# Kernel tuning notes

Measured on AMD Instinct MI355X. Metric: run time of the kernel, lower is better.

## Reference

```python
import jax, jax.numpy as jnp
import numpy as np

N, FEAT, PROP, HID, OUT = 8192, 128, 3, 256, 64
IN_SMOOTH = (PROP + 1) * FEAT  # 512
PRELU_INIT = 0.25


def prelu(x, a):
    return jnp.where(x > 0, x, a * x)


def setup_inputs() -> dict:
    key = jax.random.key(0)
    ks = jax.random.split(key, 12)
    s = 0.05
    return {
        "ori_feature": jax.random.normal(ks[0], (N, FEAT), jnp.float32),
        "smoothed_feature": jax.random.normal(ks[1], (N, IN_SMOOTH), jnp.float32),
        "processed_feature": jax.random.normal(ks[2], (N, IN_SMOOTH), jnp.float32),
        "universal_re": jax.random.normal(ks[3], (N, N), jnp.float32),
        # smooth-trans linears
        "Ws1": jax.random.normal(ks[4], (HID, IN_SMOOTH), jnp.float32) * s,
        "bs1": jnp.zeros((HID,), jnp.float32),
        "Ws2": jax.random.normal(ks[5], (OUT, HID), jnp.float32) * s,
        "bs2": jnp.zeros((OUT,), jnp.float32),
        # local-trans linears
        "Wl1": jax.random.normal(ks[6], (HID, FEAT), jnp.float32) * s,
        "bl1": jnp.zeros((HID,), jnp.float32),
        "Wl2": jax.random.normal(ks[7], (OUT, HID), jnp.float32) * s,
        "bl2": jnp.zeros((OUT,), jnp.float32),
        # hete-propagate-layer linears
        "Wh1": jax.random.normal(ks[8], (HID, IN_SMOOTH), jnp.float32) * s,
        "bh1": jnp.zeros((HID,), jnp.float32),
        "Wh2": jax.random.normal(ks[9], (OUT, HID), jnp.float32) * s,
        "bh2": jnp.zeros((OUT,), jnp.float32),
        # PReLU slopes (scalar, one per nn.PReLU())
        "a_model": jnp.float32(PRELU_INIT),
        "a_hete": jnp.float32(PRELU_INIT),
    }


def _getre_scale(emb):
    # emb: [N, OUT]
    es = jax.nn.softmax(emb, axis=1)
    re = es @ es.T                              # [N, N]
    d = jnp.diagonal(re)[:, None]               # [N, 1]
    scaling = d @ d.T                            # [N, N]
    re = re / jnp.maximum(jnp.sqrt(scaling), jnp.float32(1e-9))
    re = re - jnp.diag(jnp.diagonal(re))
    return re


def _forward(ori_feature, smoothed_feature, universal_re,
             Ws1, bs1, Ws2, bs2, Wl1, bl1, Wl2, bl2,
             Wh1, bh1, Wh2, bh2, a_model, a_hete):
    beta = jnp.float32(0.0)  # HetePropagateLayer default beta=0
    # smooth path (dropout is identity in eval)
    h = prelu(smoothed_feature @ Ws1.T + bs1, a_model)
    local_smooth_emb = h @ Ws2.T + bs2
    # local path
    g = prelu(ori_feature @ Wl1.T + bl1, a_model)
    local_ori_emb = g @ Wl2.T + bl2
    # hete propagation on input_prop_feature = smoothed_feature
    f = prelu(smoothed_feature @ Wh1.T + bh1, a_hete)
    feature_emb = f @ Wh2.T + bh2                # [N, OUT]
    re = _getre_scale(feature_emb)               # [N, N]
    lre = beta * universal_re + (1.0 - beta) * re
    m = jnp.mean(lre)
    M = jnp.max(lre)
    pos_diff = M - m                             # pos_min = 0
    shifted = lre - m
    # neg branch: -((shifted - (-m)) / (0 - (-m))) = -((shifted + m) / m)
    lre = jnp.where(shifted > 0, shifted / pos_diff, -((shifted + m) / m))
    # add_diag in source effectively adds identity to its input (bug preserved)
    lre = lre + jnp.eye(N, dtype=lre.dtype)
    pos_signal = prelu(lre, a_hete)
    neg_signal = prelu(-lre, a_hete)
    prop_pos = jax.nn.softmax(pos_signal @ feature_emb, axis=1)
    prop_neg = jax.nn.softmax(neg_signal @ feature_emb, axis=1)
    local_message_propagation = (prop_pos - prop_neg + feature_emb) / 2
    return local_ori_emb, local_smooth_emb, local_message_propagation


def reference(ori_feature, smoothed_feature, processed_feature, universal_re,
              Ws1, bs1, Ws2, bs2, Wl1, bl1, Wl2, bl2,
              Wh1, bh1, Wh2, bh2, a_model, a_hete):
    # processed_feature is unused in the original forward (only .to(device))
    return _forward(ori_feature, smoothed_feature, universal_re,
                    Ws1, bs1, Ws2, bs2, Wl1, bl1, Wl2, bl2,
                    Wh1, bh1, Wh2, bh2, a_model, a_hete)
```

## Files before the change

kernel.cpp:

```cpp
#include <hip/hip_runtime.h>
#include <hip/hip_bf16.h>

#define N 8192

typedef _Float16 half_t;
typedef __attribute__((ext_vector_type(8))) _Float16 half8;
typedef __attribute__((ext_vector_type(4))) float f32x4;
typedef unsigned int uint;
typedef unsigned short ushort;

#define MFMA16(a, b, c) __builtin_amdgcn_mfma_f32_16x16x32_f16(a, b, c, 0, 0, 0)

#define RES_SCALE 2048.0f
#define RES_INV   (1.0f / 2048.0f)

union UH8 { int4 i; half8 h; };
__device__ __forceinline__ half8 ldh(const ushort* p) {
    UH8 t; t.i = *(const int4*)p; return t.h;
}
__device__ __forceinline__ ushort h2u(half_t h) {
    union { half_t f; ushort u; } c; c.f = h; return c.u;
}

__device__ __forceinline__ float wave_max(float v) {
#pragma unroll
    for (int o = 32; o > 0; o >>= 1) v = fmaxf(v, __shfl_xor(v, o, 64));
    return v;
}
__device__ __forceinline__ float wave_sum(float v) {
#pragma unroll
    for (int o = 32; o > 0; o >>= 1) v += __shfl_xor(v, o, 64);
    return v;
}

__global__ __launch_bounds__(256) void split_f16(
    const float* __restrict__ X, ushort* __restrict__ Xh, ushort* __restrict__ Xl)
{
    const size_t i = ((size_t)blockIdx.x * 256 + threadIdx.x) * 4;
    float4 v = *(const float4*)(X + i);
    ushort h[4], l[4];
#pragma unroll
    for (int t = 0; t < 4; ++t) {
        float f = (&v.x)[t];
        half_t hh = (half_t)f;
        half_t ll = (half_t)((f - (float)hh) * RES_SCALE);
        h[t] = h2u(hh); l[t] = h2u(ll);
    }
    *(ushort4*)(Xh + i) = make_ushort4(h[0], h[1], h[2], h[3]);
    *(ushort4*)(Xl + i) = make_ushort4(l[0], l[1], l[2], l[3]);
}

__global__ __launch_bounds__(128) void gemm_f16s(
    const ushort* __restrict__ Ah, const ushort* __restrict__ Al,
    const ushort* __restrict__ Wh, const ushort* __restrict__ Wl,
    const float* __restrict__ bias, const float* __restrict__ slope_p,
    int Nc, int K, int act,
    float* __restrict__ Cf, ushort* __restrict__ Ch, ushort* __restrict__ Cl)
{
    const int w = threadIdx.x >> 6, lane = threadIdx.x & 63;
    const int l16 = lane & 15, lg = lane >> 4;
    const int row0 = blockIdx.x * 32 + w * 16;
    const int n0 = blockIdx.y * 64;
    f32x4 acc1[4], acc2[4];
#pragma unroll
    for (int c = 0; c < 4; ++c) {
        acc1[c] = (f32x4){0.f, 0.f, 0.f, 0.f};
        acc2[c] = (f32x4){0.f, 0.f, 0.f, 0.f};
    }
    for (int k0 = 0; k0 < K; k0 += 32) {
        const size_t aoff = (size_t)(row0 + l16) * K + lg * 8 + k0;
        half8 Af = ldh(Ah + aoff);
        half8 Alf = ldh(Al + aoff);
#pragma unroll
        for (int c = 0; c < 4; ++c) {
            const size_t woff = (size_t)(n0 + c * 16 + l16) * K + lg * 8 + k0;
            half8 Wf = ldh(Wh + woff);
            half8 Wlf = ldh(Wl + woff);
            acc1[c] = MFMA16(Af, Wf, acc1[c]);
            acc2[c] = MFMA16(Af, Wlf, acc2[c]);
            acc2[c] = MFMA16(Alf, Wf, acc2[c]);
        }
    }
    const float slope = *slope_p;
#pragma unroll
    for (int c = 0; c < 4; ++c) {
        const int col = n0 + c * 16 + l16;
        const float b = bias[col];
#pragma unroll
        for (int r = 0; r < 4; ++r) {
            const int row = row0 + lg * 4 + r;
            float v = fmaf(acc2[c][r], RES_INV, acc1[c][r]) + b;
            if (act) v = v > 0.f ? v : slope * v;
            const size_t off = (size_t)row * Nc + col;
            if (Cf) Cf[off] = v;
            if (Ch) {
                half_t hh = (half_t)v;
                half_t ll = (half_t)((v - (float)hh) * RES_SCALE);
                Ch[off] = h2u(hh); Cl[off] = h2u(ll);
            }
        }
    }
}

__global__ __launch_bounds__(256) void row_softmax_u(
    const float* __restrict__ E, ushort* __restrict__ uh, ushort* __restrict__ ul,
    float* __restrict__ stats)
{
    const int w = threadIdx.x >> 6, lane = threadIdx.x & 63;
    __shared__ float sacc[4][64];
    __shared__ float tacc[4];
    float s_l = 0.f, t_w = 0.f;
    const int base = blockIdx.x * 16 + w * 4;
    for (int r = 0; r < 4; ++r) {
        const int row = base + r;
        float v = E[(size_t)row * 64 + lane];
        float mx = wave_max(v);
        float e = expf(v - mx);
        float tot = wave_sum(e);
        tot = __shfl(tot, 0, 64);
        float es = e / tot;
        float dd = wave_sum(es * es);
        dd = __shfl(dd, 0, 64);
        float uv = es / sqrtf(dd);
        half_t h = (half_t)uv;
        half_t l = (half_t)((uv - (float)h) * RES_SCALE);
        const size_t idx = (size_t)row * 64 + lane;
        uh[idx] = h2u(h); ul[idx] = h2u(l);
        s_l += uv;
        float uu = wave_sum(uv * uv);
        if (lane == 0) t_w += uu;
    }
    sacc[w][lane] = s_l;
    if (lane == 0) tacc[w] = t_w;
    __syncthreads();
    if (threadIdx.x < 64) {
        float tot = sacc[0][threadIdx.x] + sacc[1][threadIdx.x] +
                    sacc[2][threadIdx.x] + sacc[3][threadIdx.x];
        atomicAdd(&stats[threadIdx.x], tot);
    }
    if (threadIdx.x == 0)
        atomicAdd(&stats[64], tacc[0] + tacc[1] + tacc[2] + tacc[3]);
}

__global__ __launch_bounds__(256) void trans_e(
    const float* __restrict__ E, ushort* __restrict__ Et)
{
    __shared__ ushort T[64][72];
    const int ib = blockIdx.x;
    const int r = threadIdx.x >> 2;
    const int c0 = (threadIdx.x & 3) * 16;
#pragma unroll
    for (int q = 0; q < 4; ++q) {
        float4 v = *(const float4*)(E + (size_t)(ib * 64 + r) * 64 + c0 + q * 4);
#pragma unroll
        for (int t = 0; t < 4; ++t)
            T[c0 + q * 4 + t][r] = h2u((half_t)((&v.x)[t]));
    }
    __syncthreads();
    const int c = threadIdx.x >> 2;
    const int j0 = (threadIdx.x & 3) * 16;
    const size_t go = (size_t)c * N + ib * 64 + j0;
    *(int4*)(Et + go)     = *(const int4*)&T[c][j0];
    *(int4*)(Et + go + 8) = *(const int4*)&T[c][j0 + 8];
}

__global__ __launch_bounds__(256) void pass_max_f16(
    const ushort* __restrict__ uh, const ushort* __restrict__ ul,
    float* __restrict__ maxbuf)
{
    const int bx = blockIdx.x;
    const int by = blockIdx.y;
    const int bid = by * 128 + bx;
    const int w = threadIdx.x >> 6, lane = threadIdx.x & 63;
    const int l16 = lane & 15, lg = lane >> 4;
    __shared__ float red[4];
    if (by * 1024 + 1024 <= bx * 64) {
        if (threadIdx.x == 0) maxbuf[bid] = 0.f;
        return;
    }
    const int i0 = bx * 64 + w * 16;
    const size_t ao = (size_t)(i0 + l16) * 64 + lg * 8;
    const half8 Ah0 = ldh(uh + ao), Ah1 = ldh(uh + ao + 32);
    const half8 Al0 = ldh(ul + ao), Al1 = ldh(ul + ao + 32);
    float mx = 0.f;
    for (int jn = 0; jn < 64; ++jn) {
        const int j0 = by * 1024 + jn * 16;
        if (j0 + 16 <= i0) continue;
        const size_t bo = (size_t)(j0 + l16) * 64 + lg * 8;
        half8 Bh0 = ldh(uh + bo), Bh1 = ldh(uh + bo + 32);
        half8 Bl0 = ldh(ul + bo), Bl1 = ldh(ul + bo + 32);
        f32x4 s1 = {0.f, 0.f, 0.f, 0.f};
        f32x4 s2 = {0.f, 0.f, 0.f, 0.f};
        s1 = MFMA16(Ah0, Bh0, s1); s1 = MFMA16(Ah1, Bh1, s1);
        s2 = MFMA16(Ah0, Bl0, s2); s2 = MFMA16(Ah1, Bl1, s2);
        s2 = MFMA16(Al0, Bh0, s2); s2 = MFMA16(Al1, Bh1, s2);
        const bool dt = (j0 == i0);
#pragma unroll
        for (int r = 0; r < 4; ++r) {
            float s = fmaf(s2[r], RES_INV, s1[r]);
            bool dg = dt && (lg * 4 + r == l16);
            mx = dg ? mx : fmaxf(mx, s);
        }
    }
    mx = wave_max(mx);
    if (lane == 0) red[w] = mx;
    __syncthreads();
    if (threadIdx.x == 0)
        maxbuf[bid] = fmaxf(fmaxf(red[0], red[1]), fmaxf(red[2], red[3]));
}

__global__ __launch_bounds__(256) void fin_m(
    const float* __restrict__ maxbuf, float* __restrict__ stats)
{
    const int t = threadIdx.x;
    float mx = 0.f;
    for (int i = t; i < 1024; i += 256) mx = fmaxf(mx, maxbuf[i]);
    mx = wave_max(mx);
    __shared__ float red[4];
    __shared__ float ssh;
    if ((t & 63) == 0) red[t >> 6] = mx;
    if (t < 64) {
        float s = stats[t];
        float ss = wave_sum(s * s);
        if (t == 0) ssh = ss;
    }
    __syncthreads();
    if (t == 0) {
        stats[65] = fmaxf(fmaxf(red[0], red[1]), fmaxf(red[2], red[3]));
        stats[66] = (ssh - stats[64]) * (1.0f / 67108864.0f);
    }
}

__global__ __launch_bounds__(256, 8) void pass_prop_f16(
    const ushort* __restrict__ uh, const ushort* __restrict__ ul,
    const ushort* __restrict__ Et, const float* __restrict__ stats,
    const float* __restrict__ ah_p, float* __restrict__ Pp, float* __restrict__ Pn)
{
    __shared__ ushort PNs[4][2][16][68];
    const int w = threadIdx.x >> 6, lane = threadIdx.x & 63;
    const int l16 = lane & 15, lg = lane >> 4;
    const int i0 = blockIdx.x * 16;
    const int js = blockIdx.y;
    const float m = stats[66];
    const float Mx = stats[65];
    const float inv_pd = 1.f / (Mx - m);
    const float c1 = -m * inv_pd;
    const float ninv_m = -1.f / m;
    const float a = *ah_p;
    const size_t ao = (size_t)(i0 + l16) * 64 + lg * 8;
    const half8 Ah0 = ldh(uh + ao), Ah1 = ldh(uh + ao + 32);
    const half8 Al0 = ldh(ul + ao), Al1 = ldh(ul + ao + 32);
    f32x4 accP[4], accN[4];
#pragma unroll
    for (int cs = 0; cs < 4; ++cs) {
        accP[cs] = (f32x4){0.f, 0.f, 0.f, 0.f};
        accN[cs] = (f32x4){0.f, 0.f, 0.f, 0.f};
    }
    ushort (*myP)[68] = PNs[w][0];
    ushort (*myN)[68] = PNs[w][1];
    for (int t = 0; t < 8; ++t) {
        const int j0 = (js * 32 + t * 4 + w) * 64;
#pragma unroll
        for (int jn = 0; jn < 4; ++jn) {
            const size_t bo = (size_t)(j0 + jn * 16 + l16) * 64 + lg * 8;
            half8 Bh0 = ldh(uh + bo), Bh1 = ldh(uh + bo + 32);
            half8 Bl0 = ldh(ul + bo), Bl1 = ldh(ul + bo + 32);
            f32x4 s1 = {0.f, 0.f, 0.f, 0.f};
            f32x4 s2 = {0.f, 0.f, 0.f, 0.f};
            s1 = MFMA16(Ah0, Bh0, s1); s1 = MFMA16(Ah1, Bh1, s1);
            s2 = MFMA16(Ah0, Bl0, s2); s2 = MFMA16(Ah1, Bl1, s2);
            s2 = MFMA16(Al0, Bh0, s2); s2 = MFMA16(Al1, Bh1, s2);
            const bool dt = (j0 + jn * 16 == i0);
#pragma unroll
            for (int r = 0; r < 4; ++r) {
                float s = fmaf(s2[r], RES_INV, s1[r]);
                float l = (s > m) ? fmaf(s, inv_pd, c1) : s * ninv_m;
                if (dt && (lg * 4 + r == l16)) l = 1.0f;
                float q = a * l;
                bool gp = l > 0.f;
                float pos = gp ? l : q;
                float neg = -(gp ? q : l);
                myP[lg * 4 + r][jn * 16 + l16] = h2u((half_t)pos);
                myN[lg * 4 + r][jn * 16 + l16] = h2u((half_t)neg);
            }
        }
#pragma unroll
        for (int kc = 0; kc < 2; ++kc) {
            const ushort* pr = &myP[l16][kc * 32 + lg * 8];
            const ushort* nr = &myN[l16][kc * 32 + lg * 8];
            UH8 tp, tn;
            *(int2*)&tp.i       = *(const int2*)pr;
            *(((int2*)&tp.i)+1) = *(const int2*)(pr + 4);
            *(int2*)&tn.i       = *(const int2*)nr;
            *(((int2*)&tn.i)+1) = *(const int2*)(nr + 4);
            const int ecol = j0 + kc * 32 + lg * 8;
#pragma unroll
            for (int cs = 0; cs < 4; ++cs) {
                const size_t eo = (size_t)(cs * 16 + l16) * N + ecol;
                half8 Ef = ldh(Et + eo);
                accP[cs] = MFMA16(tp.h, Ef, accP[cs]);
                accN[cs] = MFMA16(tn.h, Ef, accN[cs]);
            }
        }
    }
    __syncthreads();
    float* scr = (float*)&PNs[0][0][0][0];
    if (w >= 2) {
        float* base = scr + (size_t)(w - 2) * 2048;
#pragma unroll
        for (int cs = 0; cs < 4; ++cs)
#pragma unroll
            for (int r = 0; r < 4; ++r) {
                const int idx = (lg * 4 + r) * 64 + cs * 16 + l16;
                base[idx]        = accP[cs][r];
                base[idx + 1024] = accN[cs][r];
            }
    }
    __syncthreads();
    if (w < 2) {
        const float* src = scr + (size_t)w * 2048;
#pragma unroll
        for (int cs = 0; cs < 4; ++cs)
#pragma unroll
            for (int r = 0; r < 4; ++r) {
                const int idx = (lg * 4 + r) * 64 + cs * 16 + l16;
                accP[cs][r] += src[idx];
                accN[cs][r] += src[idx + 1024];
            }
    }
    __syncthreads();
    if (w == 1) {
#pragma unroll
        for (int cs = 0; cs < 4; ++cs)
#pragma unroll
            for (int r = 0; r < 4; ++r) {
                const int idx = (lg * 4 + r) * 64 + cs * 16 + l16;
                scr[idx]        = accP[cs][r];
                scr[idx + 1024] = accN[cs][r];
            }
    }
    __syncthreads();
    if (w == 0) {
#pragma unroll
        for (int cs = 0; cs < 4; ++cs)
#pragma unroll
            for (int r = 0; r < 4; ++r) {
                const int idx = (lg * 4 + r) * 64 + cs * 16 + l16;
                const size_t off = ((size_t)js * N + i0 + lg * 4 + r) * 64 + cs * 16 + l16;
                Pp[off] = accP[cs][r] + scr[idx];
                Pn[off] = accN[cs][r] + scr[idx + 1024];
            }
    }
}

__global__ __launch_bounds__(256) void fin_msg(
    const float* __restrict__ Pp, const float* __restrict__ Pn,
    const float* __restrict__ E, float* __restrict__ outm)
{
    const int w = threadIdx.x >> 6, lane = threadIdx.x & 63;
    const int row = blockIdx.x * 4 + w;
    float lp = 0.f, ln = 0.f;
#pragma unroll
    for (int js = 0; js < 4; ++js) {
        lp += Pp[((size_t)js * N + row) * 64 + lane];
        ln += Pn[((size_t)js * N + row) * 64 + lane];
    }
    float mp = wave_max(lp);
    float ep = expf(lp - mp);
    float tp = wave_sum(ep); tp = __shfl(tp, 0, 64);
    float sp = ep / tp;
    float mn = wave_max(ln);
    float en = expf(ln - mn);
    float tn = wave_sum(en); tn = __shfl(tn, 0, 64);
    float sn = en / tn;
    outm[(size_t)row * 64 + lane] = (sp - sn + E[(size_t)row * 64 + lane]) * 0.5f;
}

__global__ void init_stats(float* stats)
{
    if (threadIdx.x < 128) stats[threadIdx.x] = 0.f;
}

extern "C" void kernel_launch(void* const* d_in, const int* in_sizes, int n_in,
                              void* d_out, int out_size, void* d_ws, size_t ws_size,
                              hipStream_t stream)
{
    const float* ori = (const float*)d_in[0];
    const float* smo = (const float*)d_in[1];
    const float* Ws1 = (const float*)d_in[4];
    const float* bs1 = (const float*)d_in[5];
    const float* Ws2 = (const float*)d_in[6];
    const float* bs2 = (const float*)d_in[7];
    const float* Wl1 = (const float*)d_in[8];
    const float* bl1 = (const float*)d_in[9];
    const float* Wl2 = (const float*)d_in[10];
    const float* bl2 = (const float*)d_in[11];
    const float* Wh1 = (const float*)d_in[12];
    const float* bh1 = (const float*)d_in[13];
    const float* Wh2 = (const float*)d_in[14];
    const float* bh2 = (const float*)d_in[15];
    const float* am  = (const float*)d_in[16];
    const float* ah  = (const float*)d_in[17];

    float* out_ori = (float*)d_out;
    float* out_smo = out_ori + (size_t)N * 64;
    float* out_msg = out_smo + (size_t)N * 64;

    char* p = (char*)d_ws;
    ushort* hh    = (ushort*)p; p += (size_t)N * 256 * 2;
    ushort* hl    = (ushort*)p; p += (size_t)N * 256 * 2;
    float* E      = (float*)p;  p += (size_t)N * 64 * 4;
    float* Pp     = (float*)p;  p += (size_t)4 * N * 64 * 4;
    float* Pn     = (float*)p;  p += (size_t)4 * N * 64 * 4;
    ushort* uh    = (ushort*)p; p += (size_t)N * 64 * 2;
    ushort* ul    = (ushort*)p; p += (size_t)N * 64 * 2;
    ushort* Et    = (ushort*)p; p += (size_t)N * 64 * 2;
    ushort* orih  = (ushort*)p; p += (size_t)N * 128 * 2;
    ushort* oril  = (ushort*)p; p += (size_t)N * 128 * 2;
    ushort* Ws1h  = (ushort*)p; p += 256 * 512 * 2;
    ushort* Ws1l  = (ushort*)p; p += 256 * 512 * 2;
    ushort* Ws2h  = (ushort*)p; p += 64 * 256 * 2;
    ushort* Ws2l  = (ushort*)p; p += 64 * 256 * 2;
    ushort* Wl1h  = (ushort*)p; p += 256 * 128 * 2;
    ushort* Wl1l  = (ushort*)p; p += 256 * 128 * 2;
    ushort* Wl2h  = (ushort*)p; p += 64 * 256 * 2;
    ushort* Wl2l  = (ushort*)p; p += 64 * 256 * 2;
    ushort* Wh1h  = (ushort*)p; p += 256 * 512 * 2;
    ushort* Wh1l  = (ushort*)p; p += 256 * 512 * 2;
    ushort* Wh2h  = (ushort*)p; p += 64 * 256 * 2;
    ushort* Wh2l  = (ushort*)p; p += 64 * 256 * 2;
    float* maxbuf = (float*)p;  p += 1024 * 4;
    float* stats  = (float*)p;
    ushort* smoh = (ushort*)Pp;
    ushort* smol = (ushort*)Pn;

    const dim3 b(256);
    init_stats<<<1, 128, 0, stream>>>(stats);

    split_f16<<<4096, b, 0, stream>>>(smo, smoh, smol);
    split_f16<<<1024, b, 0, stream>>>(ori, orih, oril);
    split_f16<<<128,  b, 0, stream>>>(Ws1, Ws1h, Ws1l);
    split_f16<<<16,   b, 0, stream>>>(Ws2, Ws2h, Ws2l);
    split_f16<<<32,   b, 0, stream>>>(Wl1, Wl1h, Wl1l);
    split_f16<<<16,   b, 0, stream>>>(Wl2, Wl2h, Wl2l);
    split_f16<<<128,  b, 0, stream>>>(Wh1, Wh1h, Wh1l);
    split_f16<<<16,   b, 0, stream>>>(Wh2, Wh2h, Wh2l);

    const dim3 gb(128);
    gemm_f16s<<<dim3(256, 4), gb, 0, stream>>>(smoh, smol, Ws1h, Ws1l, bs1, am,
                                               256, 512, 1, nullptr, hh, hl);
    gemm_f16s<<<dim3(256, 1), gb, 0, stream>>>(hh, hl, Ws2h, Ws2l, bs2, am,
                                               64, 256, 0, out_smo, nullptr, nullptr);
    gemm_f16s<<<dim3(256, 4), gb, 0, stream>>>(orih, oril, Wl1h, Wl1l, bl1, am,
                                               256, 128, 1, nullptr, hh, hl);
    gemm_f16s<<<dim3(256, 1), gb, 0, stream>>>(hh, hl, Wl2h, Wl2l, bl2, am,
                                               64, 256, 0, out_ori, nullptr, nullptr);
    gemm_f16s<<<dim3(256, 4), gb, 0, stream>>>(smoh, smol, Wh1h, Wh1l, bh1, ah,
                                               256, 512, 1, nullptr, hh, hl);
    gemm_f16s<<<dim3(256, 1), gb, 0, stream>>>(hh, hl, Wh2h, Wh2l, bh2, ah,
                                               64, 256, 0, E, nullptr, nullptr);

    row_softmax_u<<<512, b, 0, stream>>>(E, uh, ul, stats);
    trans_e<<<128, b, 0, stream>>>(E, Et);
    pass_max_f16<<<dim3(128, 8), b, 0, stream>>>(uh, ul, maxbuf);
    fin_m<<<1, 256, 0, stream>>>(maxbuf, stats);
    pass_prop_f16<<<dim3(512, 4), b, 0, stream>>>(uh, ul, Et, stats, ah, Pp, Pn);
    fin_msg<<<2048, b, 0, stream>>>(Pp, Pn, E, out_msg);
}
```

Baseline: 880.0 us.

## Batch MLP GEMMs into grouped launches with split-K and fp32 second layer

The three first-layer linears now run in a single grouped launch. Each block splits K across two wave pairs and reduces the partial sums through shared memory. The three second-layer linears become one fp32 FMA kernel that reads pre-transposed weights, which removes the f16 hi/lo split of the hidden activations and of the second-layer weights. pass_prop's launch bound is also changed from 8 to 4 blocks per CU, which may allow more registers per thread. The cost is fp32 hidden buffers, which triple the workspace traffic for activations, in exchange for fewer launches and more parallelism in the small GEMMs.

```diff
diff --git a/kernel.cpp b/kernel.cpp
--- a/kernel.cpp
+++ b/kernel.cpp
@@ -50,30 +50,58 @@
     *(ushort4*)(Xl + i) = make_ushort4(l[0], l[1], l[2], l[3]);
 }
 
-__global__ __launch_bounds__(128) void gemm_f16s(
-    const ushort* __restrict__ Ah, const ushort* __restrict__ Al,
-    const ushort* __restrict__ Wh, const ushort* __restrict__ Wl,
-    const float* __restrict__ bias, const float* __restrict__ slope_p,
-    int Nc, int K, int act,
-    float* __restrict__ Cf, ushort* __restrict__ Ch, ushort* __restrict__ Cl)
-{
+__global__ __launch_bounds__(256) void trans_w2(
+    const float* __restrict__ Ws2, const float* __restrict__ Wh2,
+    const float* __restrict__ Wl2, float* __restrict__ Ts,
+    float* __restrict__ Th, float* __restrict__ Tl)
+{
+    const int z = blockIdx.y;
+    const float* in = z == 0 ? Ws2 : (z == 1 ? Wh2 : Wl2);
+    float* out = z == 0 ? Ts : (z == 1 ? Th : Tl);
+    const int idx = blockIdx.x * 256 + threadIdx.x;
+    const int k = idx >> 6, c = idx & 63;
+    out[idx] = in[c * 256 + k];
+}
+
+__global__ __launch_bounds__(256) void gemm1_f16s(
+    const ushort* __restrict__ smoh, const ushort* __restrict__ smol,
+    const ushort* __restrict__ orih, const ushort* __restrict__ oril,
+    const ushort* __restrict__ Ws1h, const ushort* __restrict__ Ws1l,
+    const ushort* __restrict__ Wh1h, const ushort* __restrict__ Wh1l,
+    const ushort* __restrict__ Wl1h, const ushort* __restrict__ Wl1l,
+    const float* __restrict__ bs1, const float* __restrict__ bh1,
+    const float* __restrict__ bl1, const float* __restrict__ am,
+    const float* __restrict__ ah,
+    float* __restrict__ h_s, float* __restrict__ h_h, float* __restrict__ h_l)
+{
+    const int z = blockIdx.z;
+    const ushort *Ah, *Al, *Wh, *Wl;
+    const float *bias, *slope;
+    float* C;
+    int K;
+    if (z == 0)      { Ah = smoh; Al = smol; Wh = Ws1h; Wl = Ws1l; bias = bs1; slope = am; C = h_s; K = 512; }
+    else if (z == 1) { Ah = smoh; Al = smol; Wh = Wh1h; Wl = Wh1l; bias = bh1; slope = ah; C = h_h; K = 512; }
+    else             { Ah = orih; Al = oril; Wh = Wl1h; Wl = Wl1l; bias = bl1; slope = am; C = h_l; K = 128; }
+    __shared__ float scr[2][16][64];
     const int w = threadIdx.x >> 6, lane = threadIdx.x & 63;
     const int l16 = lane & 15, lg = lane >> 4;
-    const int row0 = blockIdx.x * 32 + w * 16;
+    const int row0 = blockIdx.x * 32 + (w & 1) * 16;
     const int n0 = blockIdx.y * 64;
+    const int K2 = K >> 1;
+    const int koff = (w >> 1) * K2;
     f32x4 acc1[4], acc2[4];
 #pragma unroll
     for (int c = 0; c < 4; ++c) {
         acc1[c] = (f32x4){0.f, 0.f, 0.f, 0.f};
         acc2[c] = (f32x4){0.f, 0.f, 0.f, 0.f};
     }
-    for (int k0 = 0; k0 < K; k0 += 32) {
-        const size_t aoff = (size_t)(row0 + l16) * K + lg * 8 + k0;
+    for (int k0 = 0; k0 < K2; k0 += 32) {
+        const size_t aoff = (size_t)(row0 + l16) * K + koff + k0 + lg * 8;
         half8 Af = ldh(Ah + aoff);
         half8 Alf = ldh(Al + aoff);
 #pragma unroll
         for (int c = 0; c < 4; ++c) {
-            const size_t woff = (size_t)(n0 + c * 16 + l16) * K + lg * 8 + k0;
+            const size_t woff = (size_t)(n0 + c * 16 + l16) * K + koff + k0 + lg * 8;
             half8 Wf = ldh(Wh + woff);
             half8 Wlf = ldh(Wl + woff);
             acc1[c] = MFMA16(Af, Wf, acc1[c]);
@@ -81,25 +109,72 @@
             acc2[c] = MFMA16(Alf, Wf, acc2[c]);
         }
     }
-    const float slope = *slope_p;
-#pragma unroll
-    for (int c = 0; c < 4; ++c) {
-        const int col = n0 + c * 16 + l16;
-        const float b = bias[col];
+    float v[4][4];
+#pragma unroll
+    for (int c = 0; c < 4; ++c)
+#pragma unroll
+        for (int r = 0; r < 4; ++r)
+            v[c][r] = fmaf(acc2[c][r], RES_INV, acc1[c][r]);
+    if (w >= 2) {
+#pragma unroll
+        for (int c = 0; c < 4; ++c)
+#pragma unroll
+            for (int r = 0; r < 4; ++r)
+                scr[w & 1][lg * 4 + r][c * 16 + l16] = v[c][r];
+    }
+    __syncthreads();
+    if (w < 2) {
+        const float slp = *slope;
+#pragma unroll
+        for (int c = 0; c < 4; ++c) {
+            const int col = n0 + c * 16 + l16;
+            const float b = bias[col];
+#pragma unroll
+            for (int r = 0; r < 4; ++r) {
+                const int row = row0 + lg * 4 + r;
+                float val = v[c][r] + scr[w][lg * 4 + r][c * 16 + l16] + b;
+                val = val > 0.f ? val : slp * val;
+                C[(size_t)row * 256 + col] = val;
+            }
+        }
+    }
+}
+
+__global__ __launch_bounds__(256) void gemm2_val(
+    const float* __restrict__ h_s, const float* __restrict__ h_h,
+    const float* __restrict__ h_l, const float* __restrict__ Ts,
+    const float* __restrict__ Th, const float* __restrict__ Tl,
+    const float* __restrict__ bs2, const float* __restrict__ bh2,
+    const float* __restrict__ bl2, float* __restrict__ out_smo,
+    float* __restrict__ E, float* __restrict__ out_ori)
+{
+    const int z = blockIdx.y;
+    const float *h, *Wt, *bias;
+    float* out;
+    if (z == 0)      { h = h_s; Wt = Ts; bias = bs2; out = out_smo; }
+    else if (z == 1) { h = h_h; Wt = Th; bias = bh2; out = E; }
+    else             { h = h_l; Wt = Tl; bias = bl2; out = out_ori; }
+    const int w = threadIdx.x >> 6, lane = threadIdx.x & 63;
+    const int row0 = blockIdx.x * 16 + w * 4;
+    float acc[4] = {0.f, 0.f, 0.f, 0.f};
+    for (int k0 = 0; k0 < 256; k0 += 4) {
+        const float w0 = Wt[(k0 + 0) * 64 + lane];
+        const float w1 = Wt[(k0 + 1) * 64 + lane];
+        const float w2 = Wt[(k0 + 2) * 64 + lane];
+        const float w3 = Wt[(k0 + 3) * 64 + lane];
 #pragma unroll
         for (int r = 0; r < 4; ++r) {
-            const int row = row0 + lg * 4 + r;
-            float v = fmaf(acc2[c][r], RES_INV, acc1[c][r]) + b;
-            if (act) v = v > 0.f ? v : slope * v;
-            const size_t off = (size_t)row * Nc + col;
-            if (Cf) Cf[off] = v;
-            if (Ch) {
-                half_t hh = (half_t)v;
-                half_t ll = (half_t)((v - (float)hh) * RES_SCALE);
-                Ch[off] = h2u(hh); Cl[off] = h2u(ll);
-            }
+            float4 hv = *(const float4*)(h + (size_t)(row0 + r) * 256 + k0);
+            acc[r] = fmaf(hv.x, w0, acc[r]);
+            acc[r] = fmaf(hv.y, w1, acc[r]);
+            acc[r] = fmaf(hv.z, w2, acc[r]);
+            acc[r] = fmaf(hv.w, w3, acc[r]);
         }
     }
+    const float b = bias[lane];
+#pragma unroll
+    for (int r = 0; r < 4; ++r)
+        out[(size_t)(row0 + r) * 64 + lane] = acc[r] + b;
 }
 
 __global__ __launch_bounds__(256) void row_softmax_u(
@@ -231,7 +306,7 @@
     }
 }
 
-__global__ __launch_bounds__(256, 8) void pass_prop_f16(
+__global__ __launch_bounds__(256, 4) void pass_prop_f16(
     const ushort* __restrict__ uh, const ushort* __restrict__ ul,
     const ushort* __restrict__ Et, const float* __restrict__ stats,
     const float* __restrict__ ah_p, float* __restrict__ Pp, float* __restrict__ Pn)
@@ -407,8 +482,9 @@
     float* out_msg = out_smo + (size_t)N * 64;
 
     char* p = (char*)d_ws;
-    ushort* hh    = (ushort*)p; p += (size_t)N * 256 * 2;
-    ushort* hl    = (ushort*)p; p += (size_t)N * 256 * 2;
+    float* h_s    = (float*)p;  p += (size_t)N * 256 * 4;
+    float* h_h    = (float*)p;  p += (size_t)N * 256 * 4;
+    float* h_l    = (float*)p;  p += (size_t)N * 256 * 4;
     float* E      = (float*)p;  p += (size_t)N * 64 * 4;
     float* Pp     = (float*)p;  p += (size_t)4 * N * 64 * 4;
     float* Pn     = (float*)p;  p += (size_t)4 * N * 64 * 4;
@@ -419,16 +495,13 @@
     ushort* oril  = (ushort*)p; p += (size_t)N * 128 * 2;
     ushort* Ws1h  = (ushort*)p; p += 256 * 512 * 2;
     ushort* Ws1l  = (ushort*)p; p += 256 * 512 * 2;
-    ushort* Ws2h  = (ushort*)p; p += 64 * 256 * 2;
-    ushort* Ws2l  = (ushort*)p; p += 64 * 256 * 2;
+    ushort* Wh1h  = (ushort*)p; p += 256 * 512 * 2;
+    ushort* Wh1l  = (ushort*)p; p += 256 * 512 * 2;
     ushort* Wl1h  = (ushort*)p; p += 256 * 128 * 2;
     ushort* Wl1l  = (ushort*)p; p += 256 * 128 * 2;
-    ushort* Wl2h  = (ushort*)p; p += 64 * 256 * 2;
-    ushort* Wl2l  = (ushort*)p; p += 64 * 256 * 2;
-    ushort* Wh1h  = (ushort*)p; p += 256 * 512 * 2;
-    ushort* Wh1l  = (ushort*)p; p += 256 * 512 * 2;
-    ushort* Wh2h  = (ushort*)p; p += 64 * 256 * 2;
-    ushort* Wh2l  = (ushort*)p; p += 64 * 256 * 2;
+    float* W2ts   = (float*)p;  p += 256 * 64 * 4;
+    float* W2th   = (float*)p;  p += 256 * 64 * 4;
+    float* W2tl   = (float*)p;  p += 256 * 64 * 4;
     float* maxbuf = (float*)p;  p += 1024 * 4;
     float* stats  = (float*)p;
     ushort* smoh = (ushort*)Pp;
@@ -440,25 +513,15 @@
     split_f16<<<4096, b, 0, stream>>>(smo, smoh, smol);
     split_f16<<<1024, b, 0, stream>>>(ori, orih, oril);
     split_f16<<<128,  b, 0, stream>>>(Ws1, Ws1h, Ws1l);
-    split_f16<<<16,   b, 0, stream>>>(Ws2, Ws2h, Ws2l);
+    split_f16<<<128,  b, 0, stream>>>(Wh1, Wh1h, Wh1l);
     split_f16<<<32,   b, 0, stream>>>(Wl1, Wl1h, Wl1l);
-    split_f16<<<16,   b, 0, stream>>>(Wl2, Wl2h, Wl2l);
-    split_f16<<<128,  b, 0, stream>>>(Wh1, Wh1h, Wh1l);
-    split_f16<<<16,   b, 0, stream>>>(Wh2, Wh2h, Wh2l);
-
-    const dim3 gb(128);
-    gemm_f16s<<<dim3(256, 4), gb, 0, stream>>>(smoh, smol, Ws1h, Ws1l, bs1, am,
-                                               256, 512, 1, nullptr, hh, hl);
-    gemm_f16s<<<dim3(256, 1), gb, 0, stream>>>(hh, hl, Ws2h, Ws2l, bs2, am,
-                                               64, 256, 0, out_smo, nullptr, nullptr);
-    gemm_f16s<<<dim3(256, 4), gb, 0, stream>>>(orih, oril, Wl1h, Wl1l, bl1, am,
-                                               256, 128, 1, nullptr, hh, hl);
-    gemm_f16s<<<dim3(256, 1), gb, 0, stream>>>(hh, hl, Wl2h, Wl2l, bl2, am,
-                                               64, 256, 0, out_ori, nullptr, nullptr);
-    gemm_f16s<<<dim3(256, 4), gb, 0, stream>>>(smoh, smol, Wh1h, Wh1l, bh1, ah,
-                                               256, 512, 1, nullptr, hh, hl);
-    gemm_f16s<<<dim3(256, 1), gb, 0, stream>>>(hh, hl, Wh2h, Wh2l, bh2, ah,
-                                               64, 256, 0, E, nullptr, nullptr);
+    trans_w2<<<dim3(64, 3), b, 0, stream>>>(Ws2, Wh2, Wl2, W2ts, W2th, W2tl);
+
+    gemm1_f16s<<<dim3(256, 4, 3), b, 0, stream>>>(
+        smoh, smol, orih, oril, Ws1h, Ws1l, Wh1h, Wh1l, Wl1h, Wl1l,
+        bs1, bh1, bl1, am, ah, h_s, h_h, h_l);
+    gemm2_val<<<dim3(512, 3), b, 0, stream>>>(
+        h_s, h_h, h_l, W2ts, W2th, W2tl, bs2, bh2, bl2, out_smo, E, out_ori);
 
     row_softmax_u<<<512, b, 0, stream>>>(E, uh, ul, stats);
     trans_e<<<128, b, 0, stream>>>(E, Et);
```

After: 811.2 us. 1.08x faster.
